# Optimization experiments

Measured on AMD Instinct MI355X. Metric: run time of the kernel, lower is better.

Reference implementation:

```python
import jax, jax.numpy as jnp
import numpy as np

H = 128      # hidden_channels
G = 512      # number of graphs in the batch
NEG_SLOPE = 0.2


def _seg_sum(x, idx, n):
    return jax.ops.segment_sum(x, idx, num_segments=n)


def _sage(x_src, x_dst, ei, Wl, bl, Wr):
    # PyG SAGEConv: lin_l(mean_j x_j) + lin_r(x_i); lin_l has bias, lin_r does not.
    s, d = ei[0], ei[1]
    n = x_dst.shape[0]
    agg = _seg_sum(x_src[s], d, n)
    cnt = _seg_sum(jnp.ones((ei.shape[1],), x_src.dtype), d, n)
    mean = agg / jnp.maximum(cnt, 1.0)[:, None]
    return mean @ Wl + bl + x_dst @ Wr


def _gat(x_src, x_dst, ei, Ws, Wd, a_s, a_d, b):
    # PyG GATConv (heads=1, add_self_loops=False, bipartite): segment softmax over dst.
    s, d = ei[0], ei[1]
    n = x_dst.shape[0]
    hs = x_src @ Ws                                  # [N_src, H]
    hd = x_dst @ Wd                                  # [N_dst, H]
    logit = jax.nn.leaky_relu((hs @ a_s)[s] + (hd @ a_d)[d], NEG_SLOPE)
    m = jax.ops.segment_max(logit, d, num_segments=n)
    e = jnp.exp(logit - m[d])
    z = _seg_sum(e, d, n)
    alpha = e / jnp.maximum(z[d], 1e-16)
    return _seg_sum(alpha[:, None] * hs[s], d, n) + b


def _gcn(x, ei, W, b):
    # PyG GCNConv with add_self_loops=True, normalize=True (same src/dst node type).
    s, d = ei[0], ei[1]
    n = x.shape[0]
    deg = _seg_sum(jnp.ones((ei.shape[1],), x.dtype), d, n) + 1.0  # +1 self loop
    dis = jax.lax.rsqrt(deg)
    h = x @ W
    norm = dis[s] * dis[d]
    out = _seg_sum(norm[:, None] * h[s], d, n) + (dis * dis)[:, None] * h
    return out + b


def _pool(x, b):
    s = _seg_sum(x, b, G)
    c = _seg_sum(jnp.ones((x.shape[0],), x.dtype), b, G)
    return s / jnp.maximum(c, 1.0)[:, None]


def setup_inputs() -> dict:
    key = jax.random.key(0)
    ks = iter(jax.random.split(key, 80))
    scale = 1.0 / np.sqrt(H)

    def nrm(shape, sc=scale):
        return jax.random.normal(next(ks), shape, jnp.float32) * sc

    def edges(e, n_src, n_dst):
        src = jax.random.randint(next(ks), (e,), 0, n_src, jnp.int32)
        dst = jax.random.randint(next(ks), (e,), 0, n_dst, jnp.int32)
        return jnp.stack([src, dst])

    def batch(n):
        return jnp.sort(jax.random.randint(next(ks), (n,), 0, G, jnp.int32))

    N_CD, N_SEQ, N_ANNO, N_RANGE, N_MD = 100000, 80000, 80000, 80000, 50000
    inp = {
        'x_cd': nrm((N_CD, H), 1.0), 'x_seq': nrm((N_SEQ, H), 1.0),
        'x_anno': nrm((N_ANNO, H), 1.0), 'x_range': nrm((N_RANGE, H), 1.0),
        'x_md': nrm((N_MD, H), 1.0),
        'ei_seq': edges(160000, N_CD, N_SEQ),
        'ei_anno': edges(200000, N_CD, N_ANNO),
        'ei_range': edges(200000, N_CD, N_RANGE),
        'ei_comp': edges(300000, N_MD, N_CD),
        'ei_cc': edges(300000, N_CD, N_CD),
        'ei_mm': edges(150000, N_MD, N_MD),
        'b_cd': batch(N_CD), 'b_seq': batch(N_SEQ), 'b_anno': batch(N_ANNO),
        'b_range': batch(N_RANGE), 'b_md': batch(N_MD),
    }
    # per-layer stacked params (leading axis = 2 layers)
    for nm, shp in [('Wsl_seq', (2, H, H)), ('bs_seq', (2, H)), ('Wsr_seq', (2, H, H)),
                    ('Wsl_anno', (2, H, H)), ('bs_anno', (2, H)), ('Wsr_anno', (2, H, H)),
                    ('Wg_comp_s', (2, H, H)), ('Wg_comp_d', (2, H, H)),
                    ('ag_comp_s', (2, H)), ('ag_comp_d', (2, H)), ('bg_comp', (2, H)),
                    ('Wg_range_s', (2, H, H)), ('Wg_range_d', (2, H, H)),
                    ('ag_range_s', (2, H)), ('ag_range_d', (2, H)), ('bg_range', (2, H)),
                    ('Wc_cc', (2, H, H)), ('bc_cc', (2, H)),
                    ('Wc_mm', (2, H, H)), ('bc_mm', (2, H)),
                    ('lin1_W', (5 * H, H)), ('lin1_b', (H,)),
                    ('lin2_W', (H, 1)), ('lin2_b', (1,))]:
        inp[nm] = nrm(shp)
    return inp


def reference(x_cd, x_seq, x_anno, x_range, x_md,
              ei_seq, ei_anno, ei_range, ei_comp, ei_cc, ei_mm,
              b_cd, b_seq, b_anno, b_range, b_md,
              Wsl_seq, bs_seq, Wsr_seq, Wsl_anno, bs_anno, Wsr_anno,
              Wg_comp_s, Wg_comp_d, ag_comp_s, ag_comp_d, bg_comp,
              Wg_range_s, Wg_range_d, ag_range_s, ag_range_d, bg_range,
              Wc_cc, bc_cc, Wc_mm, bc_mm,
              lin1_W, lin1_b, lin2_W, lin2_b):
    for l in range(2):
        # HeteroConv aggr='sum': CD receives GAT(MD->CD) + GCN(CD->CD)
        n_cd = (_gat(x_md, x_cd, ei_comp, Wg_comp_s[l], Wg_comp_d[l],
                     ag_comp_s[l], ag_comp_d[l], bg_comp[l])
                + _gcn(x_cd, ei_cc, Wc_cc[l], bc_cc[l]))
        n_seq = _sage(x_cd, x_seq, ei_seq, Wsl_seq[l], bs_seq[l], Wsr_seq[l])
        n_anno = _sage(x_cd, x_anno, ei_anno, Wsl_anno[l], bs_anno[l], Wsr_anno[l])
        n_range = _gat(x_cd, x_range, ei_range, Wg_range_s[l], Wg_range_d[l],
                       ag_range_s[l], ag_range_d[l], bg_range[l])
        n_md = _gcn(x_md, ei_mm, Wc_mm[l], bc_mm[l])
        x_cd, x_seq, x_anno, x_range, x_md = (
            jax.nn.relu(n_cd), jax.nn.relu(n_seq), jax.nn.relu(n_anno),
            jax.nn.relu(n_range), jax.nn.relu(n_md))
    emb = jnp.concatenate([_pool(x_cd, b_cd), _pool(x_seq, b_seq),
                           _pool(x_anno, b_anno), _pool(x_range, b_range),
                           _pool(x_md, b_md)], axis=-1)        # [G, 5H]
    h = jax.nn.relu(emb @ lin1_W + lin1_b)  # Dropout(0.7) is identity in eval
    return (h @ lin2_W + lin2_b).reshape(-1)  # [G]
```

## Files before the change

kernel.cpp:

```cpp
#include <hip/hip_runtime.h>

#define HD 128
#define GNUM 512
#define RPB 520
#define IDXCAP 1024

typedef __attribute__((ext_vector_type(8))) short short8v;
typedef __attribute__((ext_vector_type(4))) float f32x4;

__device__ __forceinline__ void split1(float a, short& h, short& l) {
  unsigned u = __float_as_uint(a);
  unsigned hb = (u + 0x7FFFu + ((u >> 16) & 1u)) & 0xFFFF0000u;
  h = (short)(hb >> 16);
  float rest = a - __uint_as_float(hb);
  unsigned u2 = __float_as_uint(rest);
  l = (short)((u2 + 0x7FFFu + ((u2 >> 16) & 1u)) >> 16);
}

struct WTab { const float* p[8]; };
__global__ __launch_bounds__(256) void k_split_w(WTab tab, short* __restrict__ whi,
                                                 short* __restrict__ wlo)
{
  int m = blockIdx.x >> 6;
  int i = (blockIdx.x & 63) * 256 + threadIdx.x;
  const float* W = tab.p[m >> 1] + (m & 1) * 16384;
  int k = i >> 7, n = i & 127;
  short h, l;
  split1(W[k * 128 + n], h, l);
  whi[m * 16384 + n * 128 + k] = h;
  wlo[m * 16384 + n * 128 + k] = l;
}

#define CF_LD 132
__global__ __launch_bounds__(256) void k_gemm_mfma(
    const float* __restrict__ A1, const short* __restrict__ WH1, const short* __restrict__ WL1,
    const int* __restrict__ grp, const int* __restrict__ gcol,
    const float* __restrict__ A2, const short* __restrict__ WH2, const short* __restrict__ WL2,
    float* __restrict__ C, const float* __restrict__ bias, int N, int relu,
    const float* __restrict__ avec, float* __restrict__ adot)
{
  __shared__ char smem[64 * 136 * 2 * 2];
  __shared__ int idxbuf[IDXCAP];
  short* Ah = (short*)smem;
  short* Al = Ah + 64 * 136;
  float* Cf = (float*)smem;

  const int t = threadIdx.x;
  const int row0 = blockIdx.x * 64;
  const int lane = t & 63, wid = t >> 6;
  const int g = lane >> 4, cn = lane & 15;
  const int colbase = wid * 32;

  f32x4 zero = {0.f, 0.f, 0.f, 0.f};
  f32x4 acc[4][2];
#pragma unroll
  for (int rt = 0; rt < 4; ++rt) { acc[rt][0] = zero; acc[rt][1] = zero; }

  auto stageA = [&](const float* __restrict__ A) {
    const float4* A4 = (const float4*)(A + (size_t)row0 * 128);
#pragma unroll
    for (int i = 0; i < 8; ++i) {
      int f4 = t + i * 256;
      int row = f4 >> 5, c4 = f4 & 31;
      float4 v = make_float4(0.f, 0.f, 0.f, 0.f);
      if (row0 + row < N) v = A4[f4];
      short4 h, l;
      split1(v.x, h.x, l.x); split1(v.y, h.y, l.y);
      split1(v.z, h.z, l.z); split1(v.w, h.w, l.w);
      *(short4*)(Ah + row * 136 + c4 * 4) = h;
      *(short4*)(Al + row * 136 + c4 * 4) = l;
    }
  };

  auto stageA_gather = [&](const float* __restrict__ X, int e_lo) {
#pragma unroll
    for (int i = 0; i < 8; ++i) {
      int f4 = t + i * 256;
      int row = f4 >> 5, ln = f4 & 31;
      int r = row0 + row;
      float4 s = make_float4(0.f, 0.f, 0.f, 0.f);
      int e0 = 0, e1 = 0;
      if (r < N) { e0 = grp[r]; e1 = grp[r + 1]; }
      for (int e = e0; e < e1; ++e) {
        int off = e - e_lo;
        int c = (off < IDXCAP) ? idxbuf[off] : gcol[e];
        float4 v = *(const float4*)(X + (size_t)c * 128 + ln * 4);
        s.x += v.x; s.y += v.y; s.z += v.z; s.w += v.w;
      }
      float inv = 1.f / fmaxf((float)(e1 - e0), 1.f);
      short4 h, l;
      split1(s.x * inv, h.x, l.x); split1(s.y * inv, h.y, l.y);
      split1(s.z * inv, h.z, l.z); split1(s.w * inv, h.w, l.w);
      *(short4*)(Ah + row * 136 + ln * 4) = h;
      *(short4*)(Al + row * 136 + ln * 4) = l;
    }
  };

  auto accum = [&](const short* __restrict__ WH, const short* __restrict__ WL) {
    short8v bhi[2][4], blo[2][4];
#pragma unroll
    for (int ct = 0; ct < 2; ++ct)
#pragma unroll
      for (int kg = 0; kg < 4; ++kg) {
        size_t o = (size_t)(colbase + ct * 16 + cn) * 128 + kg * 32 + g * 8;
        bhi[ct][kg] = *(const short8v*)(WH + o);
        blo[ct][kg] = *(const short8v*)(WL + o);
      }
#pragma unroll
    for (int kg = 0; kg < 4; ++kg) {
#pragma unroll
      for (int rt = 0; rt < 4; ++rt) {
        const int ao = (rt * 16 + cn) * 136 + kg * 32 + g * 8;
        const short8v ah = *(const short8v*)(Ah + ao);
        const short8v al = *(const short8v*)(Al + ao);
#pragma unroll
        for (int ct = 0; ct < 2; ++ct) {
          acc[rt][ct] = __builtin_amdgcn_mfma_f32_16x16x32_bf16(ah, bhi[ct][kg], acc[rt][ct], 0, 0, 0);
          acc[rt][ct] = __builtin_amdgcn_mfma_f32_16x16x32_bf16(al, bhi[ct][kg], acc[rt][ct], 0, 0, 0);
          acc[rt][ct] = __builtin_amdgcn_mfma_f32_16x16x32_bf16(ah, blo[ct][kg], acc[rt][ct], 0, 0, 0);
        }
      }
    }
  };

  if (grp) {
    const int row_end = min(row0 + 64, N);
    const int e_lo = grp[row0];
    const int cnt = min(grp[row_end] - e_lo, IDXCAP);
    for (int k = t; k < cnt; k += 256) idxbuf[k] = gcol[e_lo + k];
    __syncthreads();
    stageA_gather(A1, e_lo);
  } else {
    stageA(A1);
  }
  __syncthreads();
  accum(WH1, WL1);
  if (A2) {
    __syncthreads();
    stageA(A2);
    __syncthreads();
    accum(WH2, WL2);
  }
  __syncthreads();

  if (avec) {
    float* part = (float*)smem;
    const float av0 = avec[colbase + cn];
    const float av1 = avec[colbase + 16 + cn];
#pragma unroll
    for (int rt = 0; rt < 4; ++rt)
#pragma unroll
      for (int r = 0; r < 4; ++r) {
        float p = fmaf(acc[rt][1][r], av1, acc[rt][0][r] * av0);
#pragma unroll
        for (int o = 1; o < 16; o <<= 1) p += __shfl_xor(p, o);
        if (cn == 0) part[wid * 64 + rt * 16 + g * 4 + r] = p;
      }
    __syncthreads();
    if (t < 64) {
      int row = row0 + t;
      if (row < N) adot[row] = part[t] + part[64 + t] + part[128 + t] + part[192 + t];
    }
    __syncthreads();
  }

#pragma unroll
  for (int rt = 0; rt < 4; ++rt)
#pragma unroll
    for (int ct = 0; ct < 2; ++ct)
#pragma unroll
      for (int r = 0; r < 4; ++r)
        Cf[(rt * 16 + g * 4 + r) * CF_LD + colbase + ct * 16 + cn] = acc[rt][ct][r];
  __syncthreads();

  float4* C4 = (float4*)(C + (size_t)row0 * 128);
#pragma unroll
  for (int i = 0; i < 8; ++i) {
    int f4 = t + i * 256;
    int row = f4 >> 5, c4 = f4 & 31;
    if (row0 + row < N) {
      float4 v = *(const float4*)(Cf + row * CF_LD + c4 * 4);
      if (bias) {
        float4 bv = *(const float4*)(bias + c4 * 4);
        v.x += bv.x; v.y += bv.y; v.z += bv.z; v.w += bv.w;
      }
      if (relu) {
        v.x = fmaxf(v.x, 0.f); v.y = fmaxf(v.y, 0.f);
        v.z = fmaxf(v.z, 0.f); v.w = fmaxf(v.w, 0.f);
      }
      C4[f4] = v;
    }
  }
}

__global__ void k_rowdot(const float* __restrict__ x, const float* __restrict__ a,
                         float* __restrict__ out, int N)
{
  int wid = blockIdx.x * 4 + (threadIdx.x >> 6);
  int lane = threadIdx.x & 63;
  if (wid >= N) return;
  float2 xv = ((const float2*)x)[(size_t)wid * 64 + lane];
  float2 av = ((const float2*)a)[lane];
  float v = fmaf(xv.y, av.y, xv.x * av.x);
#pragma unroll
  for (int o = 32; o > 0; o >>= 1) v += __shfl_down(v, o);
  if (lane == 0) out[wid] = v;
}

struct MTab { const float* W[4]; const float* a[4]; };
__global__ __launch_bounds__(128) void k_matvec4(MTab tb, float* __restrict__ wv)
{
  __shared__ float as[128];
  int m = blockIdx.x, i = threadIdx.x;
  as[i] = tb.a[m][i];
  __syncthreads();
  const float* W = tb.W[m];
  float v = 0.f;
  for (int j = 0; j < 128; ++j) v = fmaf(W[i * 128 + j], as[j], v);
  wv[m * 128 + i] = v;
}

struct HTab { const int* key[6]; int* cnt[6]; unsigned short* rank[6]; int bo[7]; int n[6]; };
__global__ void k_hist_rank_all(HTab tb) {
  int bi = blockIdx.x, ty = 0;
  while (ty < 5 && bi >= tb.bo[ty + 1]) ++ty;
  int i = (bi - tb.bo[ty]) * 256 + threadIdx.x;
  if (i < tb.n[ty])
    tb.rank[ty][i] = (unsigned short)atomicAdd(&tb.cnt[ty][tb.key[ty][i]], 1);
}

struct FTab { const int* es[6]; const int* ed[6]; const int* rp[6];
              const unsigned short* rank[6]; int* col[6]; int bo[7]; int n[6]; };
__global__ void k_fill_all(FTab tb) {
  int bi = blockIdx.x, ty = 0;
  while (ty < 5 && bi >= tb.bo[ty + 1]) ++ty;
  int e = (bi - tb.bo[ty]) * 256 + threadIdx.x;
  if (e >= tb.n[ty]) return;
  int p = tb.rp[ty][tb.ed[ty][e]] + (int)tb.rank[ty][e];
  tb.col[ty][p] = tb.es[ty][e];
}

struct STab { int* rp[6]; int* bs[6]; int n[6]; int bo[7]; };

__global__ __launch_bounds__(256) void k_scan_partial_all(STab tb) {
  __shared__ int red[256];
  int bi = blockIdx.x, ty = 0;
  while (ty < 5 && bi >= tb.bo[ty + 1]) ++ty;
  int lb = bi - tb.bo[ty];
  const int* rp = tb.rp[ty];
  const int N = tb.n[ty];
  const int t = threadIdx.x, base = lb * 4096;
  int s = 0;
  for (int i = t; i < 4096; i += 256) {
    int idx = base + i;
    if (idx < N) s += rp[idx];
  }
  red[t] = s;
  __syncthreads();
  for (int ofs = 128; ofs > 0; ofs >>= 1) {
    if (t < ofs) red[t] += red[t + ofs];
    __syncthreads();
  }
  if (t == 0) tb.bs[ty][lb] = red[0];
}

__global__ __launch_bounds__(256) void k_scan_bsums_all(STab tb) {
  __shared__ int sh[256];
  const int ty = blockIdx.x;
  const int nb = (tb.n[ty] + 4095) / 4096;
  const int t = threadIdx.x;
  int v = (t < nb) ? tb.bs[ty][t] : 0;
  sh[t] = v;
  __syncthreads();
  for (int ofs = 1; ofs < 256; ofs <<= 1) {
    int u = (t >= ofs) ? sh[t - ofs] : 0;
    __syncthreads();
    sh[t] += u;
    __syncthreads();
  }
  if (t < nb) tb.bs[ty][t] = sh[t] - v;
  if (t == 255) tb.rp[ty][tb.n[ty]] = sh[255];
}

__global__ __launch_bounds__(256) void k_scan_final_all(STab tb) {
  __shared__ int sh[4096 + 256];
  __shared__ int tsum[256];
  int bi = blockIdx.x, ty = 0;
  while (ty < 5 && bi >= tb.bo[ty + 1]) ++ty;
  int lb = bi - tb.bo[ty];
  int* rp = tb.rp[ty];
  const int N = tb.n[ty];
  const int t = threadIdx.x, base = lb * 4096;
  auto mp = [](int i) { return i + (i >> 4); };
#pragma unroll
  for (int i = 0; i < 16; ++i) {
    int idx = base + i * 256 + t;
    sh[mp(i * 256 + t)] = (idx < N) ? rp[idx] : 0;
  }
  __syncthreads();
  int s = 0;
#pragma unroll
  for (int j = 0; j < 16; ++j) s += sh[mp(t * 16 + j)];
  tsum[t] = s;
  __syncthreads();
  for (int ofs = 1; ofs < 256; ofs <<= 1) {
    int u = (t >= ofs) ? tsum[t - ofs] : 0;
    __syncthreads();
    tsum[t] += u;
    __syncthreads();
  }
  int pre = tsum[t] - s + tb.bs[ty][lb];
#pragma unroll
  for (int j = 0; j < 16; ++j) {
    int v = sh[mp(t * 16 + j)];
    sh[mp(t * 16 + j)] = pre;
    pre += v;
  }
  __syncthreads();
#pragma unroll
  for (int i = 0; i < 16; ++i) {
    int idx = base + i * 256 + t;
    if (idx < N) rp[idx] = sh[mp(i * 256 + t)];
  }
}

struct BTab { const int* b[5]; int n[5]; };
__global__ __launch_bounds__(512) void k_runptr(BTab tb, int* __restrict__ rpb_all) {
  const int ty = blockIdx.x;
  const int* b = tb.b[ty];
  const int N = tb.n[ty];
  const int t = threadIdx.x;
  int lo = 0, hi = N;
  while (lo < hi) {
    int mid = (lo + hi) >> 1;
    if (b[mid] < t) lo = mid + 1; else hi = mid;
  }
  rpb_all[ty * RPB + t] = lo;
  if (t == 0) rpb_all[ty * RPB + GNUM] = N;
}

struct DTab { const int* rp[2]; float* dis[2]; int n[2]; int bo[3]; };
__global__ void k_dis2(DTab tb) {
  int bi = blockIdx.x, ty = (bi >= tb.bo[1]) ? 1 : 0;
  int n = (bi - tb.bo[ty]) * 256 + threadIdx.x;
  if (n < tb.n[ty]) tb.dis[ty][n] = rsqrtf((float)(tb.rp[ty][n + 1] - tb.rp[ty][n]) + 1.f);
}

__global__ void k_gcn_gather(const int* __restrict__ rp, const int* __restrict__ col,
                             const float* __restrict__ dis, const float* __restrict__ h,
                             const float* addin, const float* __restrict__ b,
                             float* out, int N,
                             const float* __restrict__ dvec, float* __restrict__ dout)
{
  int node = blockIdx.x * 4 + (threadIdx.x >> 6);
  if (node >= N) return;
  int lane = threadIdx.x & 63;
  int s0 = rp[node], deg = rp[node + 1] - s0;
  float rd = dis[node];
  const float2* h2 = (const float2*)h;
  float2 hself = h2[(size_t)node * 64 + lane];
  float2 bv = ((const float2*)b)[lane];
  float ad0 = 0.f, ad1 = 0.f;
  if (addin) {
    float2 a2 = ((const float2*)addin)[(size_t)node * 64 + lane];
    ad0 = a2.x; ad1 = a2.y;
  }
  float a0 = 0.f, a1 = 0.f, b0 = 0.f, b1 = 0.f;
  for (int base = 0; base < deg; base += 64) {
    int m = min(64, deg - base);
    int c = 0; float dv = 0.f;
    if (lane < m) { c = col[s0 + base + lane]; dv = dis[c]; }
    int j = 0;
    for (; j + 1 < m; j += 2) {
      int sA = __shfl(c, j), sB = __shfl(c, j + 1);
      float nA = __shfl(dv, j) * rd, nB = __shfl(dv, j + 1) * rd;
      float2 vA = h2[(size_t)sA * 64 + lane];
      float2 vB = h2[(size_t)sB * 64 + lane];
      a0 = fmaf(nA, vA.x, a0); a1 = fmaf(nA, vA.y, a1);
      b0 = fmaf(nB, vB.x, b0); b1 = fmaf(nB, vB.y, b1);
    }
    if (j < m) {
      int sA = __shfl(c, j);
      float nA = __shfl(dv, j) * rd;
      float2 vA = h2[(size_t)sA * 64 + lane];
      a0 = fmaf(nA, vA.x, a0); a1 = fmaf(nA, vA.y, a1);
    }
  }
  float rr = rd * rd;
  float v0 = fmaf(rr, hself.x, a0 + b0) + bv.x + ad0;
  float v1 = fmaf(rr, hself.y, a1 + b1) + bv.y + ad1;
  v0 = fmaxf(v0, 0.f); v1 = fmaxf(v1, 0.f);
  ((float2*)out)[(size_t)node * 64 + lane] = make_float2(v0, v1);
  if (dvec) {
    float2 wv = ((const float2*)dvec)[lane];
    float p = fmaf(v1, wv.y, v0 * wv.x);
#pragma unroll
    for (int o = 32; o > 0; o >>= 1) p += __shfl_xor(p, o);
    if (lane == 0) dout[node] = p;
  }
}

__global__ void k_gat_gather(const int* __restrict__ rp, const int* __restrict__ col,
                             const float* __restrict__ hs, const float* __restrict__ as_,
                             const float* __restrict__ ad_, const float* __restrict__ b,
                             float* __restrict__ out, int N, int relu,
                             const float* __restrict__ dvec, float* __restrict__ dout)
{
  int node = blockIdx.x * 4 + (threadIdx.x >> 6);
  if (node >= N) return;
  int lane = threadIdx.x & 63;
  int s0 = rp[node], deg = rp[node + 1] - s0;
  float adn = ad_[node];
  float2 bv = ((const float2*)b)[lane];
  const float2* hs2 = (const float2*)hs;
  float z = 0.f, a0 = 0.f, a1 = 0.f, b0 = 0.f, b1 = 0.f;
  for (int base = 0; base < deg; base += 64) {
    int m = min(64, deg - base);
    int c = 0; float av = 0.f;
    if (lane < m) { c = col[s0 + base + lane]; av = as_[c]; }
    int j = 0;
    for (; j + 1 < m; j += 2) {
      int sA = __shfl(c, j), sB = __shfl(c, j + 1);
      float vA = __shfl(av, j) + adn, vB = __shfl(av, j + 1) + adn;
      vA = vA > 0.f ? vA : 0.2f * vA;
      vB = vB > 0.f ? vB : 0.2f * vB;
      float pA = __expf(vA), pB = __expf(vB);
      z += pA + pB;
      float2 hA = hs2[(size_t)sA * 64 + lane];
      float2 hB = hs2[(size_t)sB * 64 + lane];
      a0 = fmaf(pA, hA.x, a0); a1 = fmaf(pA, hA.y, a1);
      b0 = fmaf(pB, hB.x, b0); b1 = fmaf(pB, hB.y, b1);
    }
    if (j < m) {
      int sA = __shfl(c, j);
      float vA = __shfl(av, j) + adn;
      vA = vA > 0.f ? vA : 0.2f * vA;
      float pA = __expf(vA);
      z += pA;
      float2 hA = hs2[(size_t)sA * 64 + lane];
      a0 = fmaf(pA, hA.x, a0); a1 = fmaf(pA, hA.y, a1);
    }
  }
  float inv = (deg > 0) ? 1.f / z : 0.f;
  float v0 = fmaf(a0 + b0, inv, bv.x);
  float v1 = fmaf(a1 + b1, inv, bv.y);
  if (relu) { v0 = fmaxf(v0, 0.f); v1 = fmaxf(v1, 0.f); }
  ((float2*)out)[(size_t)node * 64 + lane] = make_float2(v0, v1);
  if (dvec) {
    float2 wv = ((const float2*)dvec)[lane];
    float p = fmaf(v1, wv.y, v0 * wv.x);
#pragma unroll
    for (int o = 32; o > 0; o >>= 1) p += __shfl_xor(p, o);
    if (lane == 0) dout[node] = p;
  }
}

__global__ __launch_bounds__(256) void k_pool_seg(
    const float* __restrict__ x, const int* __restrict__ rpb,
    float* __restrict__ pool, int col_off)
{
  __shared__ float2 red2[4][64];
  const int g = blockIdx.x;
  const int t = threadIdx.x, w = t >> 6, lane = t & 63;
  const int n0 = rpb[g], n1 = rpb[g + 1];
  const float2* x2 = (const float2*)x;
  float a0 = 0.f, a1 = 0.f, b0 = 0.f, b1 = 0.f;
  int n = n0 + w;
  for (; n + 4 < n1; n += 8) {
    float2 vA = x2[(size_t)n * 64 + lane];
    float2 vB = x2[(size_t)(n + 4) * 64 + lane];
    a0 += vA.x; a1 += vA.y; b0 += vB.x; b1 += vB.y;
  }
  if (n < n1) { float2 vA = x2[(size_t)n * 64 + lane]; a0 += vA.x; a1 += vA.y; }
  red2[w][lane] = make_float2(a0 + b0, a1 + b1);
  __syncthreads();
  if (t < 64) {
    float2 r0 = red2[0][t], r1 = red2[1][t], r2 = red2[2][t], r3 = red2[3][t];
    float inv = 1.f / fmaxf((float)(n1 - n0), 1.f);
    ((float2*)(pool + (size_t)g * 640 + col_off))[t] =
        make_float2((r0.x + r1.x + r2.x + r3.x) * inv,
                    (r0.y + r1.y + r2.y + r3.y) * inv);
  }
}

__global__ void k_mlp(const float* __restrict__ pool,
                      const float* __restrict__ W1, const float* __restrict__ b1,
                      const float* __restrict__ W2, const float* __restrict__ b2,
                      float* __restrict__ out)
{
  __shared__ float emb[640];
  __shared__ float red[128];
  const int g = blockIdx.x, t = threadIdx.x;
  for (int i = t; i < 640; i += 128) emb[i] = pool[(size_t)g * 640 + i];
  __syncthreads();
  float acc = b1[t];
  for (int i = 0; i < 640; ++i) acc = fmaf(emb[i], W1[i * 128 + t], acc);
  float h = fmaxf(acc, 0.f);
  red[t] = h * W2[t];
  __syncthreads();
  for (int s = 64; s > 0; s >>= 1) {
    if (t < s) red[t] += red[t + s];
    __syncthreads();
  }
  if (t == 0) out[g] = red[0] + b2[0];
}

extern "C" void kernel_launch(void* const* d_in, const int* in_sizes, int n_in,
                              void* d_out, int out_size, void* d_ws, size_t ws_size,
                              hipStream_t stream)
{
  auto fin = [&](int i) { return (const float*)d_in[i]; };
  auto iin = [&](int i) { return (const int*)d_in[i]; };

  const float *x_cd = fin(0), *x_seq = fin(1), *x_anno = fin(2), *x_range = fin(3), *x_md = fin(4);
  const int *ei_seq = iin(5), *ei_anno = iin(6), *ei_range = iin(7),
            *ei_comp = iin(8), *ei_cc = iin(9), *ei_mm = iin(10);
  const int *b_cd = iin(11), *b_seq = iin(12), *b_anno = iin(13), *b_range = iin(14), *b_md = iin(15);

  const int N_CD = in_sizes[0] / HD, N_SEQ = in_sizes[1] / HD, N_ANNO = in_sizes[2] / HD,
            N_RANGE = in_sizes[3] / HD, N_MD = in_sizes[4] / HD;
  const int E_seq = in_sizes[5] / 2, E_anno = in_sizes[6] / 2, E_range = in_sizes[7] / 2,
            E_comp = in_sizes[8] / 2, E_cc = in_sizes[9] / 2, E_mm = in_sizes[10] / 2;
  const int N_OTH = max(max(N_SEQ, N_ANNO), N_RANGE);

  auto WLm = [&](int i, int l) { return fin(i) + (size_t)l * HD * HD; };
  auto WLv = [&](int i, int l) { return fin(i) + (size_t)l * HD; };

  float* ws = (float*)d_ws;
  size_t off = 0;
  auto alloc = [&](size_t n) { float* p = ws + off; off += (n + 3) & ~(size_t)3; return p; };
  float* xcd1 = alloc((size_t)N_CD * HD);
  float* xmd1 = alloc((size_t)N_MD * HD);
  float* xoth = alloc((size_t)N_OTH * HD);
  float* acc  = alloc((size_t)N_CD * HD);
  float* t1   = alloc((size_t)N_CD * HD);
  float* sAs  = alloc((size_t)N_CD);
  float* sAd  = alloc((size_t)N_CD);
  float* sAd2 = alloc((size_t)N_CD);
  float* dis_cc = alloc((size_t)N_CD);
  float* dis_mm = alloc((size_t)N_MD);
  float* wvall = alloc(4 * HD);
  float* pool = alloc((size_t)GNUM * 5 * HD);
  short* whi = (short*)(ws + off); off += (size_t)16 * 16384 / 2;
  short* wlo = (short*)(ws + off); off += (size_t)16 * 16384 / 2;
  auto alloci = [&](size_t n) { int* p = (int*)(ws + off); off += (n + 3) & ~(size_t)3; return p; };
  int* bsall = alloci(6 * 256);
  int* rpb_all = alloci(5 * RPB);
  int Nds[6] = {N_SEQ, N_ANNO, N_RANGE, N_CD, N_CD, N_MD};
  int Es[6]  = {E_seq, E_anno, E_range, E_comp, E_cc, E_mm};
  int* rps[6];
  int* rp0 = alloci(0);
  { size_t tot = 0; for (int i = 0; i < 6; ++i) tot += (size_t)Nds[i] + 1;
    int* p = alloci(tot); rp0 = p;
    for (int i = 0; i < 6; ++i) { rps[i] = p; p += Nds[i] + 1; } }
  size_t rp_tot_bytes = 0; for (int i = 0; i < 6; ++i) rp_tot_bytes += ((size_t)Nds[i] + 1) * 4;
  unsigned short* ranks[6];
  for (int i = 0; i < 6; ++i) ranks[i] = (unsigned short*)alloci(((size_t)Es[i] + 1) / 2);
  int* cols[6];  for (int i = 0; i < 6; ++i) cols[i] = alloci((size_t)Es[i]);
  (void)n_in;

  if (off * sizeof(float) > ws_size) {
    hipMemsetAsync(d_out, 0, (size_t)out_size * sizeof(float), stream);
    return;
  }

  auto ew = [&](size_t elems) { return dim3((unsigned)((elems + 255) / 256)); };
  auto nw = [&](int N) { return dim3((unsigned)((N + 3) / 4)); };

  WTab tab;
  tab.p[0] = fin(16); tab.p[1] = fin(18); tab.p[2] = fin(19); tab.p[3] = fin(21);
  tab.p[4] = fin(22); tab.p[5] = fin(27); tab.p[6] = fin(32); tab.p[7] = fin(34);
  k_split_w<<<dim3(1024), dim3(256), 0, stream>>>(tab, whi, wlo);

  MTab mt;
  mt.W[0] = WLm(23, 0); mt.a[0] = WLv(25, 0);
  mt.W[1] = WLm(23, 1); mt.a[1] = WLv(25, 1);
  mt.W[2] = WLm(28, 0); mt.a[2] = WLv(30, 0);
  mt.W[3] = WLm(28, 1); mt.a[3] = WLv(30, 1);
  k_matvec4<<<dim3(4), dim3(128), 0, stream>>>(mt, wvall);

  {
    BTab bt;
    bt.b[0] = b_cd; bt.n[0] = N_CD;  bt.b[1] = b_seq; bt.n[1] = N_SEQ;
    bt.b[2] = b_anno; bt.n[2] = N_ANNO;  bt.b[3] = b_range; bt.n[3] = N_RANGE;
    bt.b[4] = b_md; bt.n[4] = N_MD;
    k_runptr<<<dim3(5), dim3(512), 0, stream>>>(bt, rpb_all);
  }

  const int* ess[6] = {ei_seq, ei_anno, ei_range, ei_comp, ei_cc, ei_mm};
  const int* eds[6] = {ei_seq + E_seq, ei_anno + E_anno, ei_range + E_range,
                       ei_comp + E_comp, ei_cc + E_cc, ei_mm + E_mm};
  hipMemsetAsync(rp0, 0, rp_tot_bytes, stream);
  {
    HTab ht; int b = 0;
    for (int i = 0; i < 6; ++i) {
      ht.key[i] = eds[i]; ht.cnt[i] = rps[i]; ht.rank[i] = ranks[i];
      ht.bo[i] = b; b += (Es[i] + 255) / 256; ht.n[i] = Es[i];
    }
    ht.bo[6] = b;
    k_hist_rank_all<<<dim3(b), dim3(256), 0, stream>>>(ht);
  }
  {
    STab st; int b = 0;
    for (int i = 0; i < 6; ++i) {
      st.rp[i] = rps[i]; st.bs[i] = bsall + i * 256;
      st.n[i] = Nds[i]; st.bo[i] = b; b += (Nds[i] + 4095) / 4096;
    }
    st.bo[6] = b;
    k_scan_partial_all<<<dim3(b), dim3(256), 0, stream>>>(st);
    k_scan_bsums_all<<<dim3(6), dim3(256), 0, stream>>>(st);
    k_scan_final_all<<<dim3(b), dim3(256), 0, stream>>>(st);
  }
  {
    FTab ft; int b = 0;
    for (int i = 0; i < 6; ++i) {
      ft.es[i] = ess[i]; ft.ed[i] = eds[i]; ft.rp[i] = rps[i]; ft.rank[i] = ranks[i];
      ft.col[i] = cols[i]; ft.bo[i] = b; b += (Es[i] + 255) / 256; ft.n[i] = Es[i];
    }
    ft.bo[6] = b;
    k_fill_all<<<dim3(b), dim3(256), 0, stream>>>(ft);
  }
  int *rp_seq = rps[0], *rp_anno = rps[1], *rp_range = rps[2],
      *rp_comp = rps[3], *rp_cc = rps[4], *rp_mm = rps[5];
  int *col_seq = cols[0], *col_anno = cols[1], *col_range = cols[2],
      *col_comp = cols[3], *col_cc = cols[4], *col_mm = cols[5];
  {
    DTab dt;
    dt.rp[0] = rp_cc; dt.dis[0] = dis_cc; dt.n[0] = N_CD;
    dt.rp[1] = rp_mm; dt.dis[1] = dis_mm; dt.n[1] = N_MD;
    dt.bo[0] = 0; dt.bo[1] = (N_CD + 255) / 256;
    dt.bo[2] = dt.bo[1] + (N_MD + 255) / 256;
    k_dis2<<<dim3(dt.bo[2]), dim3(256), 0, stream>>>(dt);
  }

  auto WHp = [&](int sidx, int layer) { return whi + (size_t)(sidx * 2 + layer) * 16384; };
  auto WLp = [&](int sidx, int layer) { return wlo + (size_t)(sidx * 2 + layer) * 16384; };
  auto gemm = [&](const float* A, int sidx, int layer, float* C, const float* b,
                  int N, int relu, const float* avec = nullptr, float* adot = nullptr) {
    k_gemm_mfma<<<dim3((N + 63) / 64), dim3(256), 0, stream>>>(
        A, WHp(sidx, layer), WLp(sidx, layer), nullptr, nullptr,
        nullptr, nullptr, nullptr, C, b, N, relu, avec, adot);
  };
  auto gemm2g = [&](const float* xsrc, const int* grp, const int* gcol, int s1,
                    const float* xself, int s2, int layer,
                    float* C, const float* b, int N) {
    k_gemm_mfma<<<dim3((N + 63) / 64), dim3(256), 0, stream>>>(
        xsrc, WHp(s1, layer), WLp(s1, layer), grp, gcol,
        xself, WHp(s2, layer), WLp(s2, layer), C, b, N, 1, nullptr, nullptr);
  };
  auto do_pool = [&](const float* x, int type) {
    k_pool_seg<<<dim3(GNUM), dim3(256), 0, stream>>>(x, rpb_all + type * RPB, pool, type * HD);
  };

  auto gat = [&](const float* xs, const float* xd, const int* rp, const int* col,
                 int Ns, int Nd, int sidx, int layer, const float* avs_raw,
                 const float* sAd_src, int wvD,
                 const float* dvec, float* dout,
                 const float* bias, float* out, int relu) {
    if (wvD >= 0) {
      k_rowdot<<<nw(Nd), dim3(256), 0, stream>>>(xd, wvall + wvD * 128, sAd, Nd);
      sAd_src = sAd;
    }
    gemm(xs, sidx, layer, t1, nullptr, Ns, 0, avs_raw, sAs);
    k_gat_gather<<<nw(Nd), dim3(256), 0, stream>>>(rp, col, t1, sAs, sAd_src, bias,
                                                   out, Nd, relu, dvec, dout);
  };
  auto gcn = [&](const float* x, const int* rp, const int* col, const float* dis, int N,
                 int sidx, int layer, const float* b, const float* addin, float* out,
                 const float* dvec, float* dout) {
    gemm(x, sidx, layer, t1, nullptr, N, 0);
    k_gcn_gather<<<nw(N), dim3(256), 0, stream>>>(rp, col, dis, t1, addin, b, out, N,
                                                  dvec, dout);
  };
  auto sage = [&](const float* xsrc, const float* xself, const int* rp, const int* col,
                  int Nd, int sl, int sr, int layer, const float* bl, float* out) {
    gemm2g(xsrc, rp, col, sl, xself, sr, layer, out, bl, Nd);
  };

  gat(x_md, x_cd, rp_comp, col_comp, N_MD, N_CD, 4, 0, WLv(24, 0),
      nullptr, 0, nullptr, nullptr, WLv(26, 0), acc, 0);
  gcn(x_cd, rp_cc, col_cc, dis_cc, N_CD, 6, 0, WLv(33, 0), acc, xcd1,
      wvall + 1 * 128, sAd2);
  gcn(x_md, rp_mm, col_mm, dis_mm, N_MD, 7, 0, WLv(35, 0), nullptr, xmd1,
      nullptr, nullptr);
  gat(xmd1, xcd1, rp_comp, col_comp, N_MD, N_CD, 4, 1, WLv(24, 1),
      sAd2, -1, nullptr, nullptr, WLv(26, 1), acc, 0);
  gcn(xcd1, rp_cc, col_cc, dis_cc, N_CD, 6, 1, WLv(33, 1), acc, acc,
      nullptr, nullptr);
  do_pool(acc, 0);
  gcn(xmd1, rp_mm, col_mm, dis_mm, N_MD, 7, 1, WLv(35, 1), nullptr, acc,
      nullptr, nullptr);
  do_pool(acc, 4);

  sage(x_cd, x_seq, rp_seq, col_seq, N_SEQ, 0, 1, 0, WLv(17, 0), xoth);
  sage(xcd1, xoth, rp_seq, col_seq, N_SEQ, 0, 1, 1, WLv(17, 1), acc);
  do_pool(acc, 1);
  sage(x_cd, x_anno, rp_anno, col_anno, N_ANNO, 2, 3, 0, WLv(20, 0), xoth);
  sage(xcd1, xoth, rp_anno, col_anno, N_ANNO, 2, 3, 1, WLv(20, 1), acc);
  do_pool(acc, 2);
  gat(x_cd, x_range, rp_range, col_range, N_CD, N_RANGE, 5, 0, WLv(29, 0),
      nullptr, 2, wvall + 3 * 128, sAd2, WLv(31, 0), xoth, 1);
  gat(xcd1, xoth, rp_range, col_range, N_CD, N_RANGE, 5, 1, WLv(29, 1),
      sAd2, -1, nullptr, nullptr, WLv(31, 1), acc, 1);
  do_pool(acc, 3);

  k_mlp<<<dim3(GNUM), dim3(128), 0, stream>>>(
      pool, fin(36), fin(37), fin(38), fin(39), (float*)d_out);
}
```

Baseline: 1.017 ms.

## Batch seq and anno SAGE GEMMs into one launch and prefetch self features

The seq and anno SAGE layers now run in one combined grid that dispatches blocks by index offset, so each layer needs one launch instead of two. The shared GEMM body is moved into a device function. Each block also loads its self-feature rows (A2) into registers at kernel start, which overlaps that global load with the neighbour gather and makes in-place output into the same buffer safe. In exchange, the 32 extra float registers per thread may lower occupancy, and pooling is now deferred until both types finish.

```diff
diff --git a/kernel.cpp b/kernel.cpp
--- a/kernel.cpp
+++ b/kernel.cpp
@@ -32,21 +32,20 @@
 }
 
 #define CF_LD 132
-__global__ __launch_bounds__(256) void k_gemm_mfma(
+__device__ __forceinline__ void gemm_body(
+    int blockid, char* smem, int* idxbuf,
     const float* __restrict__ A1, const short* __restrict__ WH1, const short* __restrict__ WL1,
     const int* __restrict__ grp, const int* __restrict__ gcol,
     const float* __restrict__ A2, const short* __restrict__ WH2, const short* __restrict__ WL2,
     float* __restrict__ C, const float* __restrict__ bias, int N, int relu,
     const float* __restrict__ avec, float* __restrict__ adot)
 {
-  __shared__ char smem[64 * 136 * 2 * 2];
-  __shared__ int idxbuf[IDXCAP];
   short* Ah = (short*)smem;
   short* Al = Ah + 64 * 136;
   float* Cf = (float*)smem;
 
   const int t = threadIdx.x;
-  const int row0 = blockIdx.x * 64;
+  const int row0 = blockid * 64;
   const int lane = t & 63, wid = t >> 6;
   const int g = lane >> 4, cn = lane & 15;
   const int colbase = wid * 32;
@@ -55,6 +54,17 @@
   f32x4 acc[4][2];
 #pragma unroll
   for (int rt = 0; rt < 4; ++rt) { acc[rt][0] = zero; acc[rt][1] = zero; }
+
+  float4 a2reg[8];
+  if (A2) {
+    const float4* A4 = (const float4*)(A2 + (size_t)row0 * 128);
+#pragma unroll
+    for (int i = 0; i < 8; ++i) {
+      int f4 = t + i * 256;
+      int row = f4 >> 5;
+      a2reg[i] = (row0 + row < N) ? A4[f4] : make_float4(0.f, 0.f, 0.f, 0.f);
+    }
+  }
 
   auto stageA = [&](const float* __restrict__ A) {
     const float4* A4 = (const float4*)(A + (size_t)row0 * 128);
@@ -137,7 +147,16 @@
   accum(WH1, WL1);
   if (A2) {
     __syncthreads();
-    stageA(A2);
+#pragma unroll
+    for (int i = 0; i < 8; ++i) {
+      int f4 = t + i * 256;
+      int row = f4 >> 5, c4 = f4 & 31;
+      short4 h, l;
+      split1(a2reg[i].x, h.x, l.x); split1(a2reg[i].y, h.y, l.y);
+      split1(a2reg[i].z, h.z, l.z); split1(a2reg[i].w, h.w, l.w);
+      *(short4*)(Ah + row * 136 + c4 * 4) = h;
+      *(short4*)(Al + row * 136 + c4 * 4) = l;
+    }
     __syncthreads();
     accum(WH2, WL2);
   }
@@ -191,6 +210,36 @@
       C4[f4] = v;
     }
   }
+}
+
+__global__ __launch_bounds__(256) void k_gemm_mfma(
+    const float* A1, const short* WH1, const short* WL1,
+    const int* grp, const int* gcol,
+    const float* A2, const short* WH2, const short* WL2,
+    float* C, const float* bias, int N, int relu,
+    const float* avec, float* adot)
+{
+  __shared__ char smem[64 * 136 * 2 * 2];
+  __shared__ int idxbuf[IDXCAP];
+  gemm_body(blockIdx.x, smem, idxbuf, A1, WH1, WL1, grp, gcol,
+            A2, WH2, WL2, C, bias, N, relu, avec, adot);
+}
+
+struct SPair {
+  const float* A1[2]; const short* WH1[2]; const short* WL1[2];
+  const int* grp[2]; const int* gcol[2];
+  const float* A2[2]; const short* WH2[2]; const short* WL2[2];
+  float* C[2]; const float* bias[2]; int N[2]; int bo;
+};
+__global__ __launch_bounds__(256) void k_gemm_sage2(SPair p)
+{
+  __shared__ char smem[64 * 136 * 2 * 2];
+  __shared__ int idxbuf[IDXCAP];
+  int ty = (blockIdx.x >= p.bo) ? 1 : 0;
+  int bid = blockIdx.x - (ty ? p.bo : 0);
+  gemm_body(bid, smem, idxbuf, p.A1[ty], p.WH1[ty], p.WL1[ty], p.grp[ty], p.gcol[ty],
+            p.A2[ty], p.WH2[ty], p.WL2[ty], p.C[ty], p.bias[ty], p.N[ty], 1,
+            nullptr, nullptr);
 }
 
 __global__ void k_rowdot(const float* __restrict__ x, const float* __restrict__ a,
@@ -641,12 +690,22 @@
         A, WHp(sidx, layer), WLp(sidx, layer), nullptr, nullptr,
         nullptr, nullptr, nullptr, C, b, N, relu, avec, adot);
   };
-  auto gemm2g = [&](const float* xsrc, const int* grp, const int* gcol, int s1,
-                    const float* xself, int s2, int layer,
-                    float* C, const float* b, int N) {
-    k_gemm_mfma<<<dim3((N + 63) / 64), dim3(256), 0, stream>>>(
-        xsrc, WHp(s1, layer), WLp(s1, layer), grp, gcol,
-        xself, WHp(s2, layer), WLp(s2, layer), C, b, N, 1, nullptr, nullptr);
+  auto sage2 = [&](const float* g0, const int* rp0_, const int* gc0, const float* s0,
+                   float* C0, const float* b0, int N0, int sl0, int sr0,
+                   const float* g1, const int* rp1_, const int* gc1, const float* s1,
+                   float* C1, const float* b1, int N1, int sl1, int sr1, int layer) {
+    SPair p;
+    p.A1[0] = g0; p.grp[0] = rp0_; p.gcol[0] = gc0; p.A2[0] = s0;
+    p.WH1[0] = WHp(sl0, layer); p.WL1[0] = WLp(sl0, layer);
+    p.WH2[0] = WHp(sr0, layer); p.WL2[0] = WLp(sr0, layer);
+    p.C[0] = C0; p.bias[0] = b0; p.N[0] = N0;
+    p.A1[1] = g1; p.grp[1] = rp1_; p.gcol[1] = gc1; p.A2[1] = s1;
+    p.WH1[1] = WHp(sl1, layer); p.WL1[1] = WLp(sl1, layer);
+    p.WH2[1] = WHp(sr1, layer); p.WL2[1] = WLp(sr1, layer);
+    p.C[1] = C1; p.bias[1] = b1; p.N[1] = N1;
+    p.bo = (N0 + 63) / 64;
+    int total = p.bo + (N1 + 63) / 64;
+    k_gemm_sage2<<<dim3(total), dim3(256), 0, stream>>>(p);
   };
   auto do_pool = [&](const float* x, int type) {
     k_pool_seg<<<dim3(GNUM), dim3(256), 0, stream>>>(x, rpb_all + type * RPB, pool, type * HD);
@@ -671,10 +730,6 @@
     gemm(x, sidx, layer, t1, nullptr, N, 0);
     k_gcn_gather<<<nw(N), dim3(256), 0, stream>>>(rp, col, dis, t1, addin, b, out, N,
                                                   dvec, dout);
-  };
-  auto sage = [&](const float* xsrc, const float* xself, const int* rp, const int* col,
-                  int Nd, int sl, int sr, int layer, const float* bl, float* out) {
-    gemm2g(xsrc, rp, col, sl, xself, sr, layer, out, bl, Nd);
   };
 
   gat(x_md, x_cd, rp_comp, col_comp, N_MD, N_CD, 4, 0, WLv(24, 0),
@@ -692,12 +747,13 @@
       nullptr, nullptr);
   do_pool(acc, 4);
 
-  sage(x_cd, x_seq, rp_seq, col_seq, N_SEQ, 0, 1, 0, WLv(17, 0), xoth);
-  sage(xcd1, xoth, rp_seq, col_seq, N_SEQ, 0, 1, 1, WLv(17, 1), acc);
-  do_pool(acc, 1);
-  sage(x_cd, x_anno, rp_anno, col_anno, N_ANNO, 2, 3, 0, WLv(20, 0), xoth);
-  sage(xcd1, xoth, rp_anno, col_anno, N_ANNO, 2, 3, 1, WLv(20, 1), acc);
-  do_pool(acc, 2);
+  sage2(x_cd, rp_seq, col_seq, x_seq, xoth, WLv(17, 0), N_SEQ, 0, 1,
+        x_cd, rp_anno, col_anno, x_anno, t1, WLv(20, 0), N_ANNO, 2, 3, 0);
+  sage2(xcd1, rp_seq, col_seq, xoth, xoth, WLv(17, 1), N_SEQ, 0, 1,
+        xcd1, rp_anno, col_anno, t1, t1, WLv(20, 1), N_ANNO, 2, 3, 1);
+  do_pool(xoth, 1);
+  do_pool(t1, 2);
+
   gat(x_cd, x_range, rp_range, col_range, N_CD, N_RANGE, 5, 0, WLv(29, 0),
       nullptr, 2, wvall + 3 * 128, sAd2, WLv(31, 0), xoth, 1);
   gat(xcd1, xoth, rp_range, col_range, N_CD, N_RANGE, 5, 1, WLv(29, 1),
```

Result: no change. 1.033 ms (+1.5%).
